# Performance work log

Hardware: AMD Instinct MI355X
Metric: run time of the kernel (lower is better)

The kernel has to match this reference:

```python
import jax, jax.numpy as jnp
import numpy as np
import math

N_HEADS = 8
COMPRESS = 256
ORIGIN_TOKENS = 1024
CH = 128  # per-head channels
BATCH = 32


def setup_inputs() -> dict:
    key = jax.random.key(0)
    k1, k2, k3 = jax.random.split(key, 3)
    qkv = jax.random.normal(k1, (BATCH, N_HEADS * 3 * CH, ORIGIN_TOKENS), dtype=jnp.float32)
    # nn.Linear(origin_num_tokens, compress): weight [out, in], bias [out]
    w_q = jax.random.normal(k2, (COMPRESS, ORIGIN_TOKENS), dtype=jnp.float32) * (1.0 / math.sqrt(ORIGIN_TOKENS))
    b_q = jax.random.normal(k3, (COMPRESS,), dtype=jnp.float32) * 0.01
    return {"qkv": qkv, "w_q": w_q, "b_q": b_q}


def reference(qkv, w_q, b_q):
    bs, width, length = qkv.shape
    ch = width // (3 * N_HEADS)  # per-head channels (intended semantics of source)
    # [bs, H*3*C, T] -> [bs*H, 3*C, T] -> split into q,k,v each [bs*H, C, T]
    qkv_h = qkv.reshape(bs * N_HEADS, 3 * ch, length)
    q, k, v = jnp.split(qkv_h, 3, axis=1)
    # query-compressing Linear over the token dim: [bH, C, T] -> [bH, C, compress]
    q = jnp.einsum('bct,ot->bco', q, w_q) + b_q
    scale = 1.0 / math.sqrt(math.sqrt(ch))
    # attention scores: [bH, compress, T]
    weight = jnp.einsum('bct,bcs->bts', q * scale, k * scale)
    weight = jax.nn.softmax(weight.astype(jnp.float32), axis=-1).astype(weight.dtype)
    # [bH, C, compress]
    a = jnp.einsum('bts,bcs->bct', weight, v)
    return a.reshape(bs, -1, weight.shape[1])
```

## Files before the change

### kernel.cpp

```cpp
#include <hip/hip_runtime.h>
#include <stdint.h>


namespace {

constexpr int T_ = 1024;
constexpr int SB = 32;
constexpr int NITER = T_ / SB;
constexpr float SCALE2 = 0.08838834764831845f;
constexpr float LOG2E  = 1.4426950408889634f;

typedef __bf16 bf16x8 __attribute__((ext_vector_type(8)));
typedef float  f32x4  __attribute__((ext_vector_type(4)));

constexpr int QT_OFF = 0;
constexpr int R2     = 65536;
constexpr int A_OFF  = R2;
constexpr int B_OFF  = R2 + 32768;
constexpr int KT_OFF = R2;
constexpr int VT_OFF = R2 + 16384;
constexpr int P_OFF  = R2 + 16384 + 20480;
constexpr int AL_OFF = P_OFF + 20480;
constexpr int LDS_SZ = AL_OFF + 1024;

__device__ __forceinline__ unsigned short f2bf(float f) {
    unsigned int u = __builtin_bit_cast(unsigned int, f);
    u += 0x7fffu + ((u >> 16) & 1u);
    return (unsigned short)(u >> 16);
}

__global__ __launch_bounds__(1024) void qkv_attn_kernel(
    const float* __restrict__ qkv, const float* __restrict__ wq,
    const float* __restrict__ bq, float* __restrict__ out)
{
    __shared__ alignas(16) char smem[LDS_SZ];

    const int tid  = threadIdx.x;
    const int lane = tid & 63;
    const int g    = lane >> 4;
    const int ln   = lane & 15;
    const int wv   = tid >> 6;
    const int wo   = wv << 4;

    const int wg = blockIdx.x;
    const int b  = wg >> 3, h = wg & 7;
    const float* Qg = qkv + (size_t)(b * 3072 + h * 384) * T_;
    const float* Kg = Qg + 128 * T_;
    const float* Vg = Qg + 256 * T_;

    f32x4 qacc[8];
    #pragma unroll
    for (int i = 0; i < 8; ++i) qacc[i] = f32x4{0.f, 0.f, 0.f, 0.f};

    for (int kt = 0; kt < 16; ++kt) {
        const int t0 = kt << 6;
        __syncthreads();
        #pragma unroll
        for (int j = 0; j < 4; ++j) {
            int i = tid + (j << 10);
            int row = i >> 4, t4 = i & 15;
            float4 v = *(const float4*)(wq + row * T_ + t0 + (t4 << 2));
            ushort4 hv = make_ushort4(f2bf(v.x), f2bf(v.y), f2bf(v.z), f2bf(v.w));
            *(ushort4*)(smem + A_OFF + (((row << 7) + (t4 << 3)) ^ ((row & 7) << 4))) = hv;
        }
        #pragma unroll
        for (int j = 0; j < 2; ++j) {
            int i = tid + (j << 10);
            int row = i >> 4, t4 = i & 15;
            float4 v = *(const float4*)(Qg + row * T_ + t0 + (t4 << 2));
            ushort4 hv = make_ushort4(f2bf(v.x), f2bf(v.y), f2bf(v.z), f2bf(v.w));
            *(ushort4*)(smem + B_OFF + (((row << 7) + (t4 << 3)) ^ ((row & 7) << 4))) = hv;
        }
        __syncthreads();
        #pragma unroll
        for (int kk = 0; kk < 2; ++kk) {
            int arow = wo + ln;
            bf16x8 af = *(const bf16x8*)(smem + A_OFF +
                (((arow << 7) + (kk << 6) + (g << 4)) ^ ((arow & 7) << 4)));
            #pragma unroll
            for (int ct = 0; ct < 8; ++ct) {
                int brow = (ct << 4) + ln;
                bf16x8 bfr = *(const bf16x8*)(smem + B_OFF +
                    (((brow << 7) + (kk << 6) + (g << 4)) ^ ((brow & 7) << 4)));
                qacc[ct] = __builtin_amdgcn_mfma_f32_16x16x32_bf16(af, bfr, qacc[ct], 0, 0, 0);
            }
        }
    }
    {
        float bqv[4];
        #pragma unroll
        for (int r = 0; r < 4; ++r) bqv[r] = bq[wo + (g << 2) + r];
        #pragma unroll
        for (int ct = 0; ct < 8; ++ct) {
            #pragma unroll
            for (int r = 0; r < 4; ++r) {
                int o = wo + (g << 2) + r;
                int c = (ct << 4) + ln;
                float qv = (qacc[ct][r] + bqv[r]) * SCALE2;
                *(unsigned short*)(smem + QT_OFF +
                    (((o << 8) + (c << 1)) ^ ((o & 7) << 4))) = f2bf(qv);
            }
        }
    }

    __syncthreads();

    float m_run[4], l_run[4];
    #pragma unroll
    for (int r = 0; r < 4; ++r) { m_run[r] = -1e30f; l_run[r] = 0.f; }
    f32x4 acc[8];
    #pragma unroll
    for (int i = 0; i < 8; ++i) acc[i] = f32x4{0.f, 0.f, 0.f, 0.f};

    const int sc = tid >> 3;
    const int s4 = tid & 7;
    const float* Krow = Kg + sc * T_ + (s4 << 2);
    const float* Vrow = Vg + sc * T_ + (s4 << 2);

    {
        float4 kv = *(const float4*)(Krow);
        #pragma unroll
        for (int j = 0; j < 4; ++j) {
            int srow = (s4 << 2) + j;
            *(unsigned short*)(smem + KT_OFF +
                (((srow << 8) + (sc << 1)) ^ ((srow & 7) << 4))) = f2bf((&kv.x)[j]);
        }
        float4 vv = *(const float4*)(Vrow);
        ushort4 hv = make_ushort4(f2bf(vv.x), f2bf(vv.y), f2bf(vv.z), f2bf(vv.w));
        *(ushort4*)(smem + VT_OFF + sc * 80 + (s4 << 3)) = hv;
    }

    for (int it = 0; it < NITER; ++it) {
        __syncthreads();
        const int cur = it & 1;
        if (it + 1 < NITER) {
            const int nb = cur ^ 1;
            const int s0 = (it + 1) << 5;
            float4 kv = *(const float4*)(Krow + s0);
            #pragma unroll
            for (int j = 0; j < 4; ++j) {
                int srow = (s4 << 2) + j;
                *(unsigned short*)(smem + KT_OFF + (nb << 13) +
                    (((srow << 8) + (sc << 1)) ^ ((srow & 7) << 4))) = f2bf((&kv.x)[j]);
            }
            float4 vv = *(const float4*)(Vrow + s0);
            ushort4 hv = make_ushort4(f2bf(vv.x), f2bf(vv.y), f2bf(vv.z), f2bf(vv.w));
            *(ushort4*)(smem + VT_OFF + nb * 10240 + sc * 80 + (s4 << 3)) = hv;
        }

        f32x4 L[2];
        L[0] = f32x4{0.f, 0.f, 0.f, 0.f};
        L[1] = f32x4{0.f, 0.f, 0.f, 0.f};
        #pragma unroll
        for (int kk = 0; kk < 4; ++kk) {
            int orow = wo + ln;
            bf16x8 af = *(const bf16x8*)(smem + QT_OFF +
                (((orow << 8) + (kk << 6) + (g << 4)) ^ ((orow & 7) << 4)));
            #pragma unroll
            for (int sn = 0; sn < 2; ++sn) {
                int srow = (sn << 4) + ln;
                bf16x8 bfr = *(const bf16x8*)(smem + KT_OFF + (cur << 13) +
                    (((srow << 8) + (kk << 6) + (g << 4)) ^ ((srow & 7) << 4)));
                L[sn] = __builtin_amdgcn_mfma_f32_16x16x32_bf16(af, bfr, L[sn], 0, 0, 0);
            }
        }

        float alpha;
        {
            float al[4];
            #pragma unroll
            for (int r = 0; r < 4; ++r) {
                float mx = fmaxf(L[0][r], L[1][r]);
                #pragma unroll
                for (int w = 1; w < 16; w <<= 1) mx = fmaxf(mx, __shfl_xor(mx, w, 64));
                float mnew = fmaxf(m_run[r], mx);
                float a0 = exp2f((m_run[r] - mnew) * LOG2E);
                float p0 = exp2f((L[0][r] - mnew) * LOG2E);
                float p1 = exp2f((L[1][r] - mnew) * LOG2E);
                float ts = p0 + p1;
                #pragma unroll
                for (int w = 1; w < 16; w <<= 1) ts += __shfl_xor(ts, w, 64);
                l_run[r] = l_run[r] * a0 + ts;
                m_run[r] = mnew;
                al[r] = a0;
                int o = wo + (g << 2) + r;
                *(unsigned short*)(smem + P_OFF + o * 80 + (ln << 1))      = f2bf(p0);
                *(unsigned short*)(smem + P_OFF + o * 80 + 32 + (ln << 1)) = f2bf(p1);
            }
            if (ln == 0) {
                float* alp = (float*)(smem + AL_OFF);
                #pragma unroll
                for (int r = 0; r < 4; ++r) alp[wo + (g << 2) + r] = al[r];
            }
            alpha = ((const float*)(smem + AL_OFF))[wo + ln];
        }

        #pragma unroll
        for (int mt = 0; mt < 8; ++mt) {
            acc[mt][0] *= alpha; acc[mt][1] *= alpha;
            acc[mt][2] *= alpha; acc[mt][3] *= alpha;
        }
        bf16x8 pf = *(const bf16x8*)(smem + P_OFF + (wo + ln) * 80 + (g << 4));
        #pragma unroll
        for (int mt = 0; mt < 8; ++mt) {
            int crow = (mt << 4) + ln;
            bf16x8 vf = *(const bf16x8*)(smem + VT_OFF + cur * 10240 + crow * 80 + (g << 4));
            acc[mt] = __builtin_amdgcn_mfma_f32_16x16x32_bf16(vf, pf, acc[mt], 0, 0, 0);
        }
    }

    {
        if (ln == 0) {
            float* alp = (float*)(smem + AL_OFF);
            #pragma unroll
            for (int r = 0; r < 4; ++r) alp[wo + (g << 2) + r] = l_run[r];
        }
        float linv = 1.0f / ((const float*)(smem + AL_OFF))[wo + ln];
        float* ob = out + (size_t)(b * 1024 + h * 128) * 256 + wo + ln;
        #pragma unroll
        for (int mt = 0; mt < 8; ++mt) {
            #pragma unroll
            for (int r = 0; r < 4; ++r) {
                int c = (mt << 4) + (g << 2) + r;
                ob[(size_t)c * 256] = acc[mt][r] * linv;
            }
        }
    }
}

}

extern "C" void kernel_launch(void* const* d_in, const int* in_sizes, int n_in,
                              void* d_out, int out_size, void* d_ws, size_t ws_size,
                              hipStream_t stream) {
    const float* qkv = (const float*)d_in[0];
    const float* wq  = (const float*)d_in[1];
    const float* bq  = (const float*)d_in[2];
    float* out = (float*)d_out;
    hipLaunchKernelGGL(qkv_attn_kernel, dim3(256), dim3(1024), 0, stream,
                       qkv, wq, bq, out);
}
```

Measured before the change: 600.3 us.

## Halve block to 512 threads with 32-row per-wave tiles and transposed score layout

Each wave now owns 32 compressed query rows instead of 16, so every fragment load feeds two MFMAs in the projection, score and PV stages. The score MFMA is transposed so the softmax reductions per query row become lane-local plus two cross-group shuffles. This removes the per-row shared-memory alpha exchange and its LDS array. Launch bounds now request 512 threads with 2 blocks per CU, but LDS use stays above 100KB, so two blocks may not fit together. The change also raises register pressure from the doubled accumulators.

```diff
diff --git a/kernel.cpp b/kernel.cpp
--- a/kernel.cpp
+++ b/kernel.cpp
@@ -5,8 +5,7 @@
 namespace {
 
 constexpr int T_ = 1024;
-constexpr int SB = 32;
-constexpr int NITER = T_ / SB;
+constexpr int NITER = 32;
 constexpr float SCALE2 = 0.08838834764831845f;
 constexpr float LOG2E  = 1.4426950408889634f;
 
@@ -19,9 +18,8 @@
 constexpr int B_OFF  = R2 + 32768;
 constexpr int KT_OFF = R2;
 constexpr int VT_OFF = R2 + 16384;
-constexpr int P_OFF  = R2 + 16384 + 20480;
-constexpr int AL_OFF = P_OFF + 20480;
-constexpr int LDS_SZ = AL_OFF + 1024;
+constexpr int P_OFF  = VT_OFF + 20480;
+constexpr int LDS_SZ = P_OFF + 20480;
 
 __device__ __forceinline__ unsigned short f2bf(float f) {
     unsigned int u = __builtin_bit_cast(unsigned int, f);
@@ -29,7 +27,7 @@
     return (unsigned short)(u >> 16);
 }
 
-__global__ __launch_bounds__(1024) void qkv_attn_kernel(
+__global__ __launch_bounds__(512, 2) void qkv_attn_kernel(
     const float* __restrict__ qkv, const float* __restrict__ wq,
     const float* __restrict__ bq, float* __restrict__ out)
 {
@@ -40,7 +38,7 @@
     const int g    = lane >> 4;
     const int ln   = lane & 15;
     const int wv   = tid >> 6;
-    const int wo   = wv << 4;
+    const int wo   = wv << 5;
 
     const int wg = blockIdx.x;
     const int b  = wg >> 3, h = wg & 7;
@@ -48,24 +46,26 @@
     const float* Kg = Qg + 128 * T_;
     const float* Vg = Qg + 256 * T_;
 
-    f32x4 qacc[8];
-    #pragma unroll
-    for (int i = 0; i < 8; ++i) qacc[i] = f32x4{0.f, 0.f, 0.f, 0.f};
+    f32x4 qacc[2][8];
+    #pragma unroll
+    for (int ot = 0; ot < 2; ++ot)
+        #pragma unroll
+        for (int ct = 0; ct < 8; ++ct) qacc[ot][ct] = f32x4{0.f, 0.f, 0.f, 0.f};
 
     for (int kt = 0; kt < 16; ++kt) {
         const int t0 = kt << 6;
         __syncthreads();
         #pragma unroll
-        for (int j = 0; j < 4; ++j) {
-            int i = tid + (j << 10);
+        for (int j = 0; j < 8; ++j) {
+            int i = tid + (j << 9);
             int row = i >> 4, t4 = i & 15;
             float4 v = *(const float4*)(wq + row * T_ + t0 + (t4 << 2));
             ushort4 hv = make_ushort4(f2bf(v.x), f2bf(v.y), f2bf(v.z), f2bf(v.w));
             *(ushort4*)(smem + A_OFF + (((row << 7) + (t4 << 3)) ^ ((row & 7) << 4))) = hv;
         }
         #pragma unroll
-        for (int j = 0; j < 2; ++j) {
-            int i = tid + (j << 10);
+        for (int j = 0; j < 4; ++j) {
+            int i = tid + (j << 9);
             int row = i >> 4, t4 = i & 15;
             float4 v = *(const float4*)(Qg + row * T_ + t0 + (t4 << 2));
             ushort4 hv = make_ushort4(f2bf(v.x), f2bf(v.y), f2bf(v.z), f2bf(v.w));
@@ -74,29 +74,31 @@
         __syncthreads();
         #pragma unroll
         for (int kk = 0; kk < 2; ++kk) {
-            int arow = wo + ln;
-            bf16x8 af = *(const bf16x8*)(smem + A_OFF +
-                (((arow << 7) + (kk << 6) + (g << 4)) ^ ((arow & 7) << 4)));
+            int a0r = wo + ln, a1r = wo + 16 + ln;
+            bf16x8 af0 = *(const bf16x8*)(smem + A_OFF +
+                (((a0r << 7) + (kk << 6) + (g << 4)) ^ ((a0r & 7) << 4)));
+            bf16x8 af1 = *(const bf16x8*)(smem + A_OFF +
+                (((a1r << 7) + (kk << 6) + (g << 4)) ^ ((a1r & 7) << 4)));
             #pragma unroll
             for (int ct = 0; ct < 8; ++ct) {
                 int brow = (ct << 4) + ln;
                 bf16x8 bfr = *(const bf16x8*)(smem + B_OFF +
                     (((brow << 7) + (kk << 6) + (g << 4)) ^ ((brow & 7) << 4)));
-                qacc[ct] = __builtin_amdgcn_mfma_f32_16x16x32_bf16(af, bfr, qacc[ct], 0, 0, 0);
-            }
-        }
-    }
-    {
-        float bqv[4];
-        #pragma unroll
-        for (int r = 0; r < 4; ++r) bqv[r] = bq[wo + (g << 2) + r];
-        #pragma unroll
-        for (int ct = 0; ct < 8; ++ct) {
-            #pragma unroll
-            for (int r = 0; r < 4; ++r) {
-                int o = wo + (g << 2) + r;
+                qacc[0][ct] = __builtin_amdgcn_mfma_f32_16x16x32_bf16(af0, bfr, qacc[0][ct], 0, 0, 0);
+                qacc[1][ct] = __builtin_amdgcn_mfma_f32_16x16x32_bf16(af1, bfr, qacc[1][ct], 0, 0, 0);
+            }
+        }
+    }
+    #pragma unroll
+    for (int ot = 0; ot < 2; ++ot) {
+        #pragma unroll
+        for (int r = 0; r < 4; ++r) {
+            int o = wo + (ot << 4) + (g << 2) + r;
+            float bv = bq[o];
+            #pragma unroll
+            for (int ct = 0; ct < 8; ++ct) {
                 int c = (ct << 4) + ln;
-                float qv = (qacc[ct][r] + bqv[r]) * SCALE2;
+                float qv = (qacc[ot][ct][r] + bv) * SCALE2;
                 *(unsigned short*)(smem + QT_OFF +
                     (((o << 8) + (c << 1)) ^ ((o & 7) << 4))) = f2bf(qv);
             }
@@ -105,29 +107,27 @@
 
     __syncthreads();
 
-    float m_run[4], l_run[4];
-    #pragma unroll
-    for (int r = 0; r < 4; ++r) { m_run[r] = -1e30f; l_run[r] = 0.f; }
-    f32x4 acc[8];
-    #pragma unroll
-    for (int i = 0; i < 8; ++i) acc[i] = f32x4{0.f, 0.f, 0.f, 0.f};
-
-    const int sc = tid >> 3;
+    float m_run[2] = {-1e30f, -1e30f};
+    float l_run[2] = {0.f, 0.f};
+    f32x4 acc[8][2];
+    #pragma unroll
+    for (int ct = 0; ct < 8; ++ct) { acc[ct][0] = f32x4{0,0,0,0}; acc[ct][1] = f32x4{0,0,0,0}; }
+
     const int s4 = tid & 7;
-    const float* Krow = Kg + sc * T_ + (s4 << 2);
-    const float* Vrow = Vg + sc * T_ + (s4 << 2);
-
-    {
-        float4 kv = *(const float4*)(Krow);
-        #pragma unroll
-        for (int j = 0; j < 4; ++j) {
-            int srow = (s4 << 2) + j;
+
+    #pragma unroll
+    for (int j = 0; j < 2; ++j) {
+        int c = (tid >> 3) + (j << 6);
+        float4 kv = *(const float4*)(Kg + c * T_ + (s4 << 2));
+        #pragma unroll
+        for (int jj = 0; jj < 4; ++jj) {
+            int srow = (s4 << 2) + jj;
             *(unsigned short*)(smem + KT_OFF +
-                (((srow << 8) + (sc << 1)) ^ ((srow & 7) << 4))) = f2bf((&kv.x)[j]);
-        }
-        float4 vv = *(const float4*)(Vrow);
+                (((srow << 8) + (c << 1)) ^ ((srow & 7) << 4))) = f2bf((&kv.x)[jj]);
+        }
+        float4 vv = *(const float4*)(Vg + c * T_ + (s4 << 2));
         ushort4 hv = make_ushort4(f2bf(vv.x), f2bf(vv.y), f2bf(vv.z), f2bf(vv.w));
-        *(ushort4*)(smem + VT_OFF + sc * 80 + (s4 << 3)) = hv;
+        *(ushort4*)(smem + VT_OFF + c * 80 + (s4 << 3)) = hv;
     }
 
     for (int it = 0; it < NITER; ++it) {
@@ -136,93 +136,102 @@
         if (it + 1 < NITER) {
             const int nb = cur ^ 1;
             const int s0 = (it + 1) << 5;
-            float4 kv = *(const float4*)(Krow + s0);
-            #pragma unroll
-            for (int j = 0; j < 4; ++j) {
-                int srow = (s4 << 2) + j;
-                *(unsigned short*)(smem + KT_OFF + (nb << 13) +
-                    (((srow << 8) + (sc << 1)) ^ ((srow & 7) << 4))) = f2bf((&kv.x)[j]);
-            }
-            float4 vv = *(const float4*)(Vrow + s0);
-            ushort4 hv = make_ushort4(f2bf(vv.x), f2bf(vv.y), f2bf(vv.z), f2bf(vv.w));
-            *(ushort4*)(smem + VT_OFF + nb * 10240 + sc * 80 + (s4 << 3)) = hv;
-        }
-
-        f32x4 L[2];
-        L[0] = f32x4{0.f, 0.f, 0.f, 0.f};
-        L[1] = f32x4{0.f, 0.f, 0.f, 0.f};
+            #pragma unroll
+            for (int j = 0; j < 2; ++j) {
+                int c = (tid >> 3) + (j << 6);
+                float4 kv = *(const float4*)(Kg + c * T_ + s0 + (s4 << 2));
+                #pragma unroll
+                for (int jj = 0; jj < 4; ++jj) {
+                    int srow = (s4 << 2) + jj;
+                    *(unsigned short*)(smem + KT_OFF + (nb << 13) +
+                        (((srow << 8) + (c << 1)) ^ ((srow & 7) << 4))) = f2bf((&kv.x)[jj]);
+                }
+                float4 vv = *(const float4*)(Vg + c * T_ + s0 + (s4 << 2));
+                ushort4 hv = make_ushort4(f2bf(vv.x), f2bf(vv.y), f2bf(vv.z), f2bf(vv.w));
+                *(ushort4*)(smem + VT_OFF + nb * 10240 + c * 80 + (s4 << 3)) = hv;
+            }
+        }
+
+        f32x4 L[2][2];
+        L[0][0] = f32x4{0,0,0,0}; L[0][1] = f32x4{0,0,0,0};
+        L[1][0] = f32x4{0,0,0,0}; L[1][1] = f32x4{0,0,0,0};
         #pragma unroll
         for (int kk = 0; kk < 4; ++kk) {
-            int orow = wo + ln;
-            bf16x8 af = *(const bf16x8*)(smem + QT_OFF +
-                (((orow << 8) + (kk << 6) + (g << 4)) ^ ((orow & 7) << 4)));
+            int s0r = ln, s1r = 16 + ln;
+            bf16x8 ak0 = *(const bf16x8*)(smem + KT_OFF + (cur << 13) +
+                (((s0r << 8) + (kk << 6) + (g << 4)) ^ ((s0r & 7) << 4)));
+            bf16x8 ak1 = *(const bf16x8*)(smem + KT_OFF + (cur << 13) +
+                (((s1r << 8) + (kk << 6) + (g << 4)) ^ ((s1r & 7) << 4)));
+            int o0r = wo + ln, o1r = wo + 16 + ln;
+            bf16x8 bq0 = *(const bf16x8*)(smem + QT_OFF +
+                (((o0r << 8) + (kk << 6) + (g << 4)) ^ ((o0r & 7) << 4)));
+            bf16x8 bq1 = *(const bf16x8*)(smem + QT_OFF +
+                (((o1r << 8) + (kk << 6) + (g << 4)) ^ ((o1r & 7) << 4)));
+            L[0][0] = __builtin_amdgcn_mfma_f32_16x16x32_bf16(ak0, bq0, L[0][0], 0, 0, 0);
+            L[0][1] = __builtin_amdgcn_mfma_f32_16x16x32_bf16(ak0, bq1, L[0][1], 0, 0, 0);
+            L[1][0] = __builtin_amdgcn_mfma_f32_16x16x32_bf16(ak1, bq0, L[1][0], 0, 0, 0);
+            L[1][1] = __builtin_amdgcn_mfma_f32_16x16x32_bf16(ak1, bq1, L[1][1], 0, 0, 0);
+        }
+
+        float alpha[2];
+        #pragma unroll
+        for (int ot = 0; ot < 2; ++ot) {
+            float mx = fmaxf(fmaxf(fmaxf(L[0][ot][0], L[0][ot][1]), fmaxf(L[0][ot][2], L[0][ot][3])),
+                             fmaxf(fmaxf(L[1][ot][0], L[1][ot][1]), fmaxf(L[1][ot][2], L[1][ot][3])));
+            mx = fmaxf(mx, __shfl_xor(mx, 16, 64));
+            mx = fmaxf(mx, __shfl_xor(mx, 32, 64));
+            float mnew = fmaxf(m_run[ot], mx);
+            float a0 = exp2f((m_run[ot] - mnew) * LOG2E);
+            float ts = 0.f;
+            ushort4 pw[2];
             #pragma unroll
             for (int sn = 0; sn < 2; ++sn) {
-                int srow = (sn << 4) + ln;
-                bf16x8 bfr = *(const bf16x8*)(smem + KT_OFF + (cur << 13) +
-                    (((srow << 8) + (kk << 6) + (g << 4)) ^ ((srow & 7) << 4)));
-                L[sn] = __builtin_amdgcn_mfma_f32_16x16x32_bf16(af, bfr, L[sn], 0, 0, 0);
-            }
-        }
-
-        float alpha;
-        {
-            float al[4];
+                float p0 = exp2f((L[sn][ot][0] - mnew) * LOG2E);
+                float p1 = exp2f((L[sn][ot][1] - mnew) * LOG2E);
+                float p2 = exp2f((L[sn][ot][2] - mnew) * LOG2E);
+                float p3 = exp2f((L[sn][ot][3] - mnew) * LOG2E);
+                ts += (p0 + p1) + (p2 + p3);
+                pw[sn] = make_ushort4(f2bf(p0), f2bf(p1), f2bf(p2), f2bf(p3));
+            }
+            ts += __shfl_xor(ts, 16, 64);
+            ts += __shfl_xor(ts, 32, 64);
+            l_run[ot] = l_run[ot] * a0 + ts;
+            m_run[ot] = mnew;
+            alpha[ot] = a0;
+            char* pr = smem + P_OFF + (wo + (ot << 4) + ln) * 80;
+            *(ushort4*)(pr + ((g << 2) << 1))        = pw[0];
+            *(ushort4*)(pr + ((16 + (g << 2)) << 1)) = pw[1];
+        }
+
+        #pragma unroll
+        for (int ct = 0; ct < 8; ++ct) {
+            #pragma unroll
+            for (int ot = 0; ot < 2; ++ot) {
+                acc[ct][ot][0] *= alpha[ot]; acc[ct][ot][1] *= alpha[ot];
+                acc[ct][ot][2] *= alpha[ot]; acc[ct][ot][3] *= alpha[ot];
+            }
+        }
+        bf16x8 pf0 = *(const bf16x8*)(smem + P_OFF + (wo + ln) * 80 + (g << 4));
+        bf16x8 pf1 = *(const bf16x8*)(smem + P_OFF + (wo + 16 + ln) * 80 + (g << 4));
+        #pragma unroll
+        for (int ct = 0; ct < 8; ++ct) {
+            int c = (ct << 4) + ln;
+            bf16x8 vf = *(const bf16x8*)(smem + VT_OFF + cur * 10240 + c * 80 + (g << 4));
+            acc[ct][0] = __builtin_amdgcn_mfma_f32_16x16x32_bf16(vf, pf0, acc[ct][0], 0, 0, 0);
+            acc[ct][1] = __builtin_amdgcn_mfma_f32_16x16x32_bf16(vf, pf1, acc[ct][1], 0, 0, 0);
+        }
+    }
+
+    {
+        float linv0 = 1.0f / l_run[0], linv1 = 1.0f / l_run[1];
+        float* ob = out + ((size_t)b * 1024 + h * 128) * 256;
+        #pragma unroll
+        for (int ct = 0; ct < 8; ++ct) {
             #pragma unroll
             for (int r = 0; r < 4; ++r) {
-                float mx = fmaxf(L[0][r], L[1][r]);
-                #pragma unroll
-                for (int w = 1; w < 16; w <<= 1) mx = fmaxf(mx, __shfl_xor(mx, w, 64));
-                float mnew = fmaxf(m_run[r], mx);
-                float a0 = exp2f((m_run[r] - mnew) * LOG2E);
-                float p0 = exp2f((L[0][r] - mnew) * LOG2E);
-                float p1 = exp2f((L[1][r] - mnew) * LOG2E);
-                float ts = p0 + p1;
-                #pragma unroll
-                for (int w = 1; w < 16; w <<= 1) ts += __shfl_xor(ts, w, 64);
-                l_run[r] = l_run[r] * a0 + ts;
-                m_run[r] = mnew;
-                al[r] = a0;
-                int o = wo + (g << 2) + r;
-                *(unsigned short*)(smem + P_OFF + o * 80 + (ln << 1))      = f2bf(p0);
-                *(unsigned short*)(smem + P_OFF + o * 80 + 32 + (ln << 1)) = f2bf(p1);
-            }
-            if (ln == 0) {
-                float* alp = (float*)(smem + AL_OFF);
-                #pragma unroll
-                for (int r = 0; r < 4; ++r) alp[wo + (g << 2) + r] = al[r];
-            }
-            alpha = ((const float*)(smem + AL_OFF))[wo + ln];
-        }
-
-        #pragma unroll
-        for (int mt = 0; mt < 8; ++mt) {
-            acc[mt][0] *= alpha; acc[mt][1] *= alpha;
-            acc[mt][2] *= alpha; acc[mt][3] *= alpha;
-        }
-        bf16x8 pf = *(const bf16x8*)(smem + P_OFF + (wo + ln) * 80 + (g << 4));
-        #pragma unroll
-        for (int mt = 0; mt < 8; ++mt) {
-            int crow = (mt << 4) + ln;
-            bf16x8 vf = *(const bf16x8*)(smem + VT_OFF + cur * 10240 + crow * 80 + (g << 4));
-            acc[mt] = __builtin_amdgcn_mfma_f32_16x16x32_bf16(vf, pf, acc[mt], 0, 0, 0);
-        }
-    }
-
-    {
-        if (ln == 0) {
-            float* alp = (float*)(smem + AL_OFF);
-            #pragma unroll
-            for (int r = 0; r < 4; ++r) alp[wo + (g << 2) + r] = l_run[r];
-        }
-        float linv = 1.0f / ((const float*)(smem + AL_OFF))[wo + ln];
-        float* ob = out + (size_t)(b * 1024 + h * 128) * 256 + wo + ln;
-        #pragma unroll
-        for (int mt = 0; mt < 8; ++mt) {
-            #pragma unroll
-            for (int r = 0; r < 4; ++r) {
-                int c = (mt << 4) + (g << 2) + r;
-                ob[(size_t)c * 256] = acc[mt][r] * linv;
+                int c = (ct << 4) + (g << 2) + r;
+                ob[(size_t)c * 256 + wo + ln]      = acc[ct][0][r] * linv0;
+                ob[(size_t)c * 256 + wo + 16 + ln] = acc[ct][1][r] * linv1;
             }
         }
     }
@@ -237,6 +246,6 @@
     const float* wq  = (const float*)d_in[1];
     const float* bq  = (const float*)d_in[2];
     float* out = (float*)d_out;
-    hipLaunchKernelGGL(qkv_attn_kernel, dim3(256), dim3(1024), 0, stream,
+    hipLaunchKernelGGL(qkv_attn_kernel, dim3(256), dim3(512), 0, stream,
                        qkv, wq, bq, out);
 }
```

Result: no change. 595.2 us (-0.8%).
